# Optimization experiments

Measured on AMD Instinct MI355X. Metric: run time of the kernel, lower is better.

The kernel has to match this reference:

```python
import jax, jax.numpy as jnp
import numpy as np

# --- hash-grid hyperparameters (from module source) ---
N_LEVELS = 16
F_PER_LEVEL = 2
LOG2_T = 19
TABLE_SIZE = 1 << LOG2_T           # 524288 entries per level
BASE_RES = 16
PER_LEVEL_SCALE = 1.447269237440378
N_NEURONS = 64
N_OUT = 3

# per-level grid resolutions (static python ints)
SCALES = np.floor(BASE_RES * PER_LEVEL_SCALE ** np.arange(N_LEVELS)).astype(np.float32)

# spatial hash primes for 2D (tiny-cuda-nn convention)
PRIME0 = np.uint32(1)
PRIME1 = np.uint32(2654435761)
HASH_MASK = np.uint32(TABLE_SIZE - 1)

# 4 bilinear corner offsets for 2D
CORNERS = np.array([[0, 0], [0, 1], [1, 0], [1, 1]], dtype=np.int32)  # [4,2]


def setup_inputs() -> dict:
    key = jax.random.key(0)
    k_pts, k_tab, k_w1, k_w2 = jax.random.split(key, 4)
    N = 1 << 20
    points = jax.random.uniform(k_pts, (N, 2), dtype=jnp.float32)
    # tcnn initializes hash features uniform in [-1e-4, 1e-4]
    table = jax.random.uniform(k_tab, (N_LEVELS, TABLE_SIZE, F_PER_LEVEL),
                               dtype=jnp.float32, minval=-1e-4, maxval=1e-4)
    d_enc = N_LEVELS * F_PER_LEVEL  # 32
    # bias-free VanillaMLP: 32 -> 64 (ReLU) -> 3
    W1 = jax.random.normal(k_w1, (N_NEURONS, d_enc), dtype=jnp.float32) * (1.0 / np.sqrt(d_enc))
    W2 = jax.random.normal(k_w2, (N_OUT, N_NEURONS), dtype=jnp.float32) * (1.0 / np.sqrt(N_NEURONS))
    return {"points": points, "table": table, "W1": W1, "W2": W2}


def hash_encode(points, table):
    # points: [N,2] in [0,1]; table: [L,T,F]
    scales = jnp.asarray(SCALES)                        # [L]
    pos = points[None, :, :] * scales[:, None, None]    # [L,N,2]
    p0 = jnp.floor(pos)
    frac = pos - p0                                     # [L,N,2]
    base = p0.astype(jnp.int32)                         # [L,N,2]
    corners = jnp.asarray(CORNERS)                      # [4,2]
    coords = base[:, :, None, :] + corners[None, None]  # [L,N,4,2]
    cu = coords.astype(jnp.uint32)
    h = (cu[..., 0] * PRIME0) ^ (cu[..., 1] * PRIME1)   # [L,N,4] uint32
    idx = (h & HASH_MASK).astype(jnp.int32)             # [L,N,4]
    L, N = idx.shape[0], idx.shape[1]
    # gather features: [L, N*4, F]
    feats = jnp.take_along_axis(table, idx.reshape(L, N * 4, 1), axis=1)
    feats = feats.reshape(L, N, 4, F_PER_LEVEL)
    # bilinear weights: prod over dims of (frac if corner bit else 1-frac)
    cbit = corners[None, None].astype(frac.dtype)        # [1,1,4,2]
    w = jnp.prod(jnp.where(cbit == 1.0, frac[:, :, None, :], 1.0 - frac[:, :, None, :]), axis=-1)  # [L,N,4]
    interp = jnp.einsum('lnc,lncf->lnf', w, feats)       # [L,N,F]
    # level-major concat per point -> [N, L*F]
    return interp.transpose(1, 0, 2).reshape(N, L * F_PER_LEVEL)


def reference(points, table, W1, W2):
    enc = hash_encode(points, table)                     # [N,32]
    h = jax.nn.relu(enc @ W1.T)                          # [N,64]
    rgbs = h @ W2.T                                      # [N,3]
    return rgbs
```

## Files before the change

kernel.cpp:

```cpp
#include <hip/hip_runtime.h>
#include <math.h>

#define NLV 16
#define TBL (1u << 19)
#define HMASK (TBL - 1u)
#define PRIME1 2654435761u

#define BINSHIFT 7
#define BINW (1 << BINSHIFT)
#define NBINS (BINW * BINW)
#define CAP 64
#define NSEG 512
#define SEGCAP 512
#define OVF3CAP 1024
#define NB4 (NBINS / 4)

struct Scales { float s[NLV]; };

typedef float vf2 __attribute__((ext_vector_type(2)));

__device__ __forceinline__ void pk_fma(vf2& acc, vf2 a, vf2 w) {
    asm("v_pk_fma_f32 %0, %1, %2, %0" : "+v"(acc) : "v"(a), "s"(w));
}

__device__ __forceinline__ int point_bin(float2 p) {
    int bx = (int)(p.x * (float)BINW);
    int by = (int)(p.y * (float)BINW);
    return (by << BINSHIFT) + bx;
}

__device__ __forceinline__ void process_point(
    int i, float2 p,
    const float2* __restrict__ table,
    const float*  __restrict__ W1,
    const float*  __restrict__ W2,
    float* __restrict__ out,
    const Scales& sc)
{
    vf2 enc2[16];
#pragma unroll
    for (int l = 0; l < NLV; ++l) {
        float s  = sc.s[l];
        float px = p.x * s;
        float py = p.y * s;
        float fpx = floorf(px), fpy = floorf(py);
        float fx = px - fpx, fy = py - fpy;
        unsigned bx = (unsigned)(int)fpx;
        unsigned by = (unsigned)(int)fpy;
        unsigned hy0 = by * PRIME1;
        unsigned hy1 = hy0 + PRIME1;
        const float2* tl = table + (size_t)l * TBL;
        float2 f00 = tl[( bx        ^ hy0) & HMASK];
        float2 f01 = tl[( bx        ^ hy1) & HMASK];
        float2 f10 = tl[((bx + 1u)  ^ hy0) & HMASK];
        float2 f11 = tl[((bx + 1u)  ^ hy1) & HMASK];
        float gx = 1.f - fx, gy = 1.f - fy;
        float w00 = gx * gy, w01 = gx * fy, w10 = fx * gy, w11 = fx * fy;
        float ex = w00*f00.x + w01*f01.x + w10*f10.x + w11*f11.x;
        float ey = w00*f00.y + w01*f01.y + w10*f10.y + w11*f11.y;
        enc2[l] = (vf2){ex, ey};
    }

    const vf2* w1v = (const vf2*)W1;
    float o0 = 0.f, o1 = 0.f, o2 = 0.f;
#pragma unroll
    for (int n = 0; n < 64; ++n) {
        vf2 hp0 = {0.f, 0.f}, hp1 = {0.f, 0.f};
#pragma unroll
        for (int k = 0; k < 8; ++k) {
            pk_fma(hp0, enc2[2*k],     w1v[n*16 + 2*k]);
            pk_fma(hp1, enc2[2*k + 1], w1v[n*16 + 2*k + 1]);
        }
        float h = (hp0.x + hp0.y) + (hp1.x + hp1.y);
        h = fmaxf(h, 0.f);
        o0 = fmaf(h, W2[      n], o0);
        o1 = fmaf(h, W2[ 64 + n], o1);
        o2 = fmaf(h, W2[128 + n], o2);
    }
    out[3*i + 0] = o0;
    out[3*i + 1] = o1;
    out[3*i + 2] = o2;
}

__global__ void fill_kernel(const float2* __restrict__ pts,
                            int* __restrict__ cnt, int* __restrict__ cnt2,
                            int* __restrict__ ovf3cnt,
                            int* __restrict__ bucket, int* __restrict__ seglist,
                            int* __restrict__ ovf3, int N) {
    int i = blockIdx.x * 256 + threadIdx.x;
    if (i >= N) return;
    int b = point_bin(pts[i]);
    int pos = atomicAdd(&cnt[b], 1);
    if (pos < CAP) {
        bucket[b * CAP + pos] = i;
    } else {
        int seg = b >> 5;
        int p2 = atomicAdd(&cnt2[seg * 16], 1);
        if (p2 < SEGCAP) seglist[seg * SEGCAP + p2] = i;
        else {
            int p3 = atomicAdd(ovf3cnt, 1);
            if (p3 < OVF3CAP) ovf3[p3] = i;
        }
    }
}

__global__ __launch_bounds__(256, 4) void hashgrid_mlp_main(
    const float2* __restrict__ pts,
    const float2* __restrict__ table,
    const int*    __restrict__ cnt,
    const int*    __restrict__ cnt2,
    const int*    __restrict__ ovf3cnt,
    const int*    __restrict__ bucket,
    const int*    __restrict__ seglist,
    const int*    __restrict__ ovf3,
    const float*  __restrict__ W1,
    const float*  __restrict__ W2,
    float* __restrict__ out, Scales sc)
{
    int bid = blockIdx.x;
    int tid = threadIdx.x;
    int i = -1;
    if (bid < NB4) {
        int bin  = bid * 4 + (tid >> 6);
        int slot = tid & 63;
        int c = cnt[bin];
        if (c > CAP) c = CAP;
        if (slot < c) i = bucket[bin * CAP + slot];
    } else if (bid < NB4 + 2 * NSEG) {
        int sidx = bid - NB4;
        int seg  = sidx >> 1;
        int t    = (sidx & 1) * 256 + tid;
        int c = cnt2[seg * 16];
        if (c > SEGCAP) c = SEGCAP;
        if (t < c) i = seglist[seg * SEGCAP + t];
    } else {
        int t = (bid - NB4 - 2 * NSEG) * 256 + tid;
        int c = *ovf3cnt;
        if (c > OVF3CAP) c = OVF3CAP;
        if (t < c) i = ovf3[t];
    }
    if (i >= 0) process_point(i, pts[i], table, W1, W2, out, sc);
}

__global__ __launch_bounds__(256, 4) void hashgrid_mlp_fallback(
    const float2* __restrict__ pts, const float2* __restrict__ table,
    const float* __restrict__ W1, const float* __restrict__ W2,
    float* __restrict__ out, int N, Scales sc)
{
    int i = blockIdx.x * 256 + threadIdx.x;
    if (i >= N) return;
    process_point(i, pts[i], table, W1, W2, out, sc);
}

extern "C" void kernel_launch(void* const* d_in, const int* in_sizes, int n_in,
                              void* d_out, int out_size, void* d_ws, size_t ws_size,
                              hipStream_t stream) {
    const float2* pts   = (const float2*)d_in[0];
    const float2* table = (const float2*)d_in[1];
    const float*  W1    = (const float*)d_in[2];
    const float*  W2    = (const float*)d_in[3];
    float* out = (float*)d_out;
    int N = in_sizes[0] / 2;

    Scales sc;
    for (int l = 0; l < NLV; ++l)
        sc.s[l] = (float)floor(16.0 * pow(1.447269237440378, (double)l));

    int blocks = (N + 255) / 256;

    size_t need = ((size_t)NBINS + NSEG * 16 + 16 + OVF3CAP +
                   (size_t)NSEG * SEGCAP + (size_t)NBINS * CAP) * sizeof(int);

    if (ws_size >= need) {
        int* cnt     = (int*)d_ws;
        int* cnt2    = cnt + NBINS;
        int* ovf3cnt = cnt2 + NSEG * 16;
        int* ovf3    = ovf3cnt + 16;
        int* seglist = ovf3 + OVF3CAP;
        int* bucket  = seglist + (size_t)NSEG * SEGCAP;
        hipMemsetAsync(cnt, 0, ((size_t)NBINS + NSEG * 16 + 16) * sizeof(int),
                       stream);
        hipLaunchKernelGGL(fill_kernel, dim3(blocks), dim3(256), 0, stream,
                           pts, cnt, cnt2, ovf3cnt, bucket, seglist, ovf3, N);
        hipLaunchKernelGGL(hashgrid_mlp_main,
                           dim3(NB4 + 2 * NSEG + 4), dim3(256), 0, stream,
                           pts, table, cnt, cnt2, ovf3cnt, bucket, seglist, ovf3,
                           W1, W2, out, sc);
    } else {
        hipLaunchKernelGGL(hashgrid_mlp_fallback, dim3(blocks), dim3(256), 0, stream,
                           pts, table, W1, W2, out, N, sc);
    }
}
```

Baseline: 171.1 us.

## Stage coarse-level hash table corners in LDS per spatial bucket block

For bucketed blocks, which cover a 4x1 strip of spatial bins, the first 11 levels' grid corners covering the block's region are gathered from the hash table into shared memory cooperatively. Each point then reads its bilinear corners from LDS instead of issuing global gathers for those levels. This targets the redundant random global gathers that points in the same region repeat at coarse resolutions. It adds a staging pass, a __syncthreads and about 6KB of LDS per block. It also relies on the staged window bounds always containing each point's cells, which is not checked.

```diff
diff --git a/kernel.cpp b/kernel.cpp
--- a/kernel.cpp
+++ b/kernel.cpp
@@ -15,6 +15,12 @@
 #define OVF3CAP 1024
 #define NB4 (NBINS / 4)
 
+#define NSTG 11
+#define STOT 763
+__device__ __constant__ const int SW[NSTG]   = {5,5,6,6,7,8,9,11,14,18,24};
+__device__ __constant__ const int SH[NSTG]   = {5,5,5,5,5,5,6,6,7,8,9};
+__device__ __constant__ const int SOFF[NSTG] = {0,25,50,80,110,145,185,239,305,403,547};
+
 struct Scales { float s[NLV]; };
 
 typedef float vf2 __attribute__((ext_vector_type(2)));
@@ -30,7 +36,8 @@
 }
 
 __device__ __forceinline__ void process_point(
-    int i, float2 p,
+    int i, float2 p, bool use_lds, float x0f, float y0f,
+    const float2* sd,
     const float2* __restrict__ table,
     const float*  __restrict__ W1,
     const float*  __restrict__ W2,
@@ -45,15 +52,27 @@
         float py = p.y * s;
         float fpx = floorf(px), fpy = floorf(py);
         float fx = px - fpx, fy = py - fpy;
-        unsigned bx = (unsigned)(int)fpx;
-        unsigned by = (unsigned)(int)fpy;
-        unsigned hy0 = by * PRIME1;
-        unsigned hy1 = hy0 + PRIME1;
-        const float2* tl = table + (size_t)l * TBL;
-        float2 f00 = tl[( bx        ^ hy0) & HMASK];
-        float2 f01 = tl[( bx        ^ hy1) & HMASK];
-        float2 f10 = tl[((bx + 1u)  ^ hy0) & HMASK];
-        float2 f11 = tl[((bx + 1u)  ^ hy1) & HMASK];
+        float2 f00, f01, f10, f11;
+        if (l < NSTG && use_lds) {
+            int bx = (int)fpx, by = (int)fpy;
+            int cx0 = (int)floorf(x0f * s) - 1;
+            int cy0 = (int)floorf(y0f * s) - 1;
+            int base = SOFF[l] + (by - cy0) * SW[l] + (bx - cx0);
+            f00 = sd[base];
+            f10 = sd[base + 1];
+            f01 = sd[base + SW[l]];
+            f11 = sd[base + SW[l] + 1];
+        } else {
+            unsigned bx = (unsigned)(int)fpx;
+            unsigned by = (unsigned)(int)fpy;
+            unsigned hy0 = by * PRIME1;
+            unsigned hy1 = hy0 + PRIME1;
+            const float2* tl = table + (size_t)l * TBL;
+            f00 = tl[( bx        ^ hy0) & HMASK];
+            f01 = tl[( bx        ^ hy1) & HMASK];
+            f10 = tl[((bx + 1u)  ^ hy0) & HMASK];
+            f11 = tl[((bx + 1u)  ^ hy1) & HMASK];
+        }
         float gx = 1.f - fx, gy = 1.f - fy;
         float w00 = gx * gy, w01 = gx * fy, w10 = fx * gy, w11 = fx * fy;
         float ex = w00*f00.x + w01*f01.x + w10*f10.x + w11*f11.x;
@@ -117,10 +136,13 @@
     const float*  __restrict__ W2,
     float* __restrict__ out, Scales sc)
 {
+    __shared__ float2 sd[STOT];
     int bid = blockIdx.x;
     int tid = threadIdx.x;
+    bool bucketblk = bid < NB4;
+
     int i = -1;
-    if (bid < NB4) {
+    if (bucketblk) {
         int bin  = bid * 4 + (tid >> 6);
         int slot = tid & 63;
         int c = cnt[bin];
@@ -139,7 +161,33 @@
         if (c > OVF3CAP) c = OVF3CAP;
         if (t < c) i = ovf3[t];
     }
-    if (i >= 0) process_point(i, pts[i], table, W1, W2, out, sc);
+
+    float x0f = 0.f, y0f = 0.f;
+    if (bucketblk) {
+        int b0 = bid * 4;
+        int X0 = b0 & (BINW - 1), Y0 = b0 >> BINSHIFT;
+        x0f = (float)X0 * 0.0078125f;
+        y0f = (float)Y0 * 0.0078125f;
+#pragma unroll
+        for (int l = 0; l < NSTG; ++l) {
+            float s = sc.s[l];
+            int cx0 = (int)floorf(x0f * s) - 1;
+            int cy0 = (int)floorf(y0f * s) - 1;
+            const float2* tl = table + (size_t)l * TBL;
+            const int n = SW[l] * SH[l];
+            for (int e = tid; e < n; e += 256) {
+                int cx = cx0 + e % SW[l];
+                int cy = cy0 + e / SW[l];
+                unsigned h = ((unsigned)cx ^ ((unsigned)cy * PRIME1)) & HMASK;
+                sd[SOFF[l] + e] = tl[h];
+            }
+        }
+    }
+    __syncthreads();
+
+    if (i >= 0)
+        process_point(i, pts[i], bucketblk, x0f, y0f, sd,
+                      table, W1, W2, out, sc);
 }
 
 __global__ __launch_bounds__(256, 4) void hashgrid_mlp_fallback(
@@ -147,9 +195,10 @@
     const float* __restrict__ W1, const float* __restrict__ W2,
     float* __restrict__ out, int N, Scales sc)
 {
+    __shared__ float2 dummy[1];
     int i = blockIdx.x * 256 + threadIdx.x;
     if (i >= N) return;
-    process_point(i, pts[i], table, W1, W2, out, sc);
+    process_point(i, pts[i], false, 0.f, 0.f, dummy, table, W1, W2, out, sc);
 }
 
 extern "C" void kernel_launch(void* const* d_in, const int* in_sizes, int n_in,
```

Result: slower. 215.8 us (+26.1%).

## Stage coarse-level hash cells per bin in registers and fetch via wave shuffles

Applied to the files above, without the earlier changes.

In bucket blocks, lanes 0-15 of each wavefront preload the 4x4 neighbourhood of hash-table features around the bin for the 8 coarsest levels. Each point then gets its bilinear corners for those levels with __shfl instead of scattered global loads. The aim is to cut cache and memory traffic for the coarse levels. In exchange it adds many cross-lane permute instructions, extra registers, and reliance on the bin-to-cell geometry and float floor consistency for correctness.

```diff
diff --git a/kernel.cpp b/kernel.cpp
--- a/kernel.cpp
+++ b/kernel.cpp
@@ -14,6 +14,7 @@
 #define SEGCAP 512
 #define OVF3CAP 1024
 #define NB4 (NBINS / 4)
+#define NPERM 8
 
 struct Scales { float s[NLV]; };
 
@@ -30,7 +31,8 @@
 }
 
 __device__ __forceinline__ void process_point(
-    int i, float2 p,
+    int i, float2 p, bool staged, float x0f, float y0f,
+    const float2* cellv,
     const float2* __restrict__ table,
     const float*  __restrict__ W1,
     const float*  __restrict__ W2,
@@ -45,15 +47,31 @@
         float py = p.y * s;
         float fpx = floorf(px), fpy = floorf(py);
         float fx = px - fpx, fy = py - fpy;
-        unsigned bx = (unsigned)(int)fpx;
-        unsigned by = (unsigned)(int)fpy;
-        unsigned hy0 = by * PRIME1;
-        unsigned hy1 = hy0 + PRIME1;
-        const float2* tl = table + (size_t)l * TBL;
-        float2 f00 = tl[( bx        ^ hy0) & HMASK];
-        float2 f01 = tl[( bx        ^ hy1) & HMASK];
-        float2 f10 = tl[((bx + 1u)  ^ hy0) & HMASK];
-        float2 f11 = tl[((bx + 1u)  ^ hy1) & HMASK];
+        float2 f00, f01, f10, f11;
+        if (l < NPERM && staged) {
+            int bx = (int)fpx, by = (int)fpy;
+            int cx0 = (int)floorf(x0f * s);
+            int cy0 = (int)floorf(y0f * s);
+            int sel = ((by - cy0) << 2) + (bx - cx0);
+            f00.x = __shfl(cellv[l].x, sel,     64);
+            f00.y = __shfl(cellv[l].y, sel,     64);
+            f10.x = __shfl(cellv[l].x, sel + 1, 64);
+            f10.y = __shfl(cellv[l].y, sel + 1, 64);
+            f01.x = __shfl(cellv[l].x, sel + 4, 64);
+            f01.y = __shfl(cellv[l].y, sel + 4, 64);
+            f11.x = __shfl(cellv[l].x, sel + 5, 64);
+            f11.y = __shfl(cellv[l].y, sel + 5, 64);
+        } else {
+            unsigned bx = (unsigned)(int)fpx;
+            unsigned by = (unsigned)(int)fpy;
+            unsigned hy0 = by * PRIME1;
+            unsigned hy1 = hy0 + PRIME1;
+            const float2* tl = table + (size_t)l * TBL;
+            f00 = tl[( bx        ^ hy0) & HMASK];
+            f01 = tl[( bx        ^ hy1) & HMASK];
+            f10 = tl[((bx + 1u)  ^ hy0) & HMASK];
+            f11 = tl[((bx + 1u)  ^ hy1) & HMASK];
+        }
         float gx = 1.f - fx, gy = 1.f - fy;
         float w00 = gx * gy, w01 = gx * fy, w10 = fx * gy, w11 = fx * fy;
         float ex = w00*f00.x + w01*f01.x + w10*f10.x + w11*f11.x;
@@ -119,9 +137,12 @@
 {
     int bid = blockIdx.x;
     int tid = threadIdx.x;
+    bool bucketblk = bid < NB4;
+
     int i = -1;
-    if (bid < NB4) {
-        int bin  = bid * 4 + (tid >> 6);
+    int bin = 0;
+    if (bucketblk) {
+        bin = bid * 4 + (tid >> 6);
         int slot = tid & 63;
         int c = cnt[bin];
         if (c > CAP) c = CAP;
@@ -139,7 +160,31 @@
         if (c > OVF3CAP) c = OVF3CAP;
         if (t < c) i = ovf3[t];
     }
-    if (i >= 0) process_point(i, pts[i], table, W1, W2, out, sc);
+
+    float x0f = 0.f, y0f = 0.f;
+    float2 cellv[NPERM];
+    if (bucketblk) {
+        x0f = (float)(bin & (BINW - 1)) * 0.0078125f;
+        y0f = (float)(bin >> BINSHIFT)  * 0.0078125f;
+        int t  = tid & 63;
+        int tx = t & 3, ty = t >> 2;
+#pragma unroll
+        for (int l = 0; l < NPERM; ++l) {
+            float s = sc.s[l];
+            int cx0 = (int)floorf(x0f * s);
+            int cy0 = (int)floorf(y0f * s);
+            if (t < 16) {
+                unsigned cx = (unsigned)(cx0 + tx);
+                unsigned cy = (unsigned)(cy0 + ty);
+                unsigned h = (cx ^ (cy * PRIME1)) & HMASK;
+                cellv[l] = table[(size_t)l * TBL + h];
+            }
+        }
+    }
+
+    if (i >= 0)
+        process_point(i, pts[i], bucketblk, x0f, y0f, cellv,
+                      table, W1, W2, out, sc);
 }
 
 __global__ __launch_bounds__(256, 4) void hashgrid_mlp_fallback(
@@ -147,9 +192,10 @@
     const float* __restrict__ W1, const float* __restrict__ W2,
     float* __restrict__ out, int N, Scales sc)
 {
+    float2 dummy[NPERM];
     int i = blockIdx.x * 256 + threadIdx.x;
     if (i >= N) return;
-    process_point(i, pts[i], table, W1, W2, out, sc);
+    process_point(i, pts[i], false, 0.f, 0.f, dummy, table, W1, W2, out, sc);
 }
 
 extern "C" void kernel_launch(void* const* d_in, const int* in_sizes, int n_in,
```

Measured after the change: 181.8 us. +6.2%, slower.
